# Optimization experiments

Hardware: AMD Instinct MI355X
Metric: run time of the kernel (lower is better)

Reference implementation:

```python
import jax, jax.numpy as jnp
import numpy as np

H, DK = 8, 64  # n_head, d_k (= d_v)
LN_EPS = 1e-6


def _layer_norm(x, g, b):
    mu = jnp.mean(x, axis=-1, keepdims=True)
    var = jnp.var(x, axis=-1, keepdims=True)
    return (x - mu) * jax.lax.rsqrt(var + LN_EPS) * g + b


def setup_inputs() -> dict:
    key = jax.random.key(0)
    ks = jax.random.split(key, 8)
    B, S, D, DF = 8, 1024, 512, 2048
    s = 0.02
    return {
        "enc_input": jax.random.normal(ks[0], (B, S, D), jnp.float32),
        "cost_mat": jax.random.normal(ks[1], (B, S, S), jnp.float32),
        "wq": jax.random.normal(ks[2], (D, D), jnp.float32) * s,
        "wk": jax.random.normal(ks[3], (D, D), jnp.float32) * s,
        "wv": jax.random.normal(ks[4], (D, D), jnp.float32) * s,
        "fc_w": jax.random.normal(ks[5], (D, D), jnp.float32) * s,
        "ln1_g": jnp.ones((D,), jnp.float32),
        "ln1_b": jnp.zeros((D,), jnp.float32),
        "w1": jax.random.normal(ks[6], (DF, D), jnp.float32) * s,
        "b1": jnp.zeros((DF,), jnp.float32),
        "w2": jax.random.normal(ks[7], (D, DF), jnp.float32) * s,
        "b2": jnp.zeros((D,), jnp.float32),
        "ln2_g": jnp.ones((D,), jnp.float32),
        "ln2_b": jnp.zeros((D,), jnp.float32),
    }


def reference(enc_input, cost_mat, wq, wk, wv, fc_w, ln1_g, ln1_b,
              w1, b1, w2, b2, ln2_g, ln2_b):
    B, S, D = enc_input.shape
    # Q/K/V projections -> [B, H, S, dk]
    q = (enc_input @ wq.T).reshape(B, S, H, DK).transpose(0, 2, 1, 3)
    k = (enc_input @ wk.T).reshape(B, S, H, DK).transpose(0, 2, 1, 3)
    v = (enc_input @ wv.T).reshape(B, S, H, DK).transpose(0, 2, 1, 3)
    # mixed score: scaled QK^T plus cost matrix broadcast over heads
    scores = jnp.einsum("bhqd,bhkd->bhqk", q, k) / np.sqrt(DK).astype(np.float32)
    scores = scores + cost_mat[:, None, :, :]
    attn = jax.nn.softmax(scores, axis=-1)
    ctx = jnp.einsum("bhqk,bhkd->bhqd", attn, v)  # [B,H,S,dk]
    ctx = ctx.transpose(0, 2, 1, 3).reshape(B, S, D)
    attn_out = _layer_norm(ctx @ fc_w.T + enc_input, ln1_g, ln1_b)
    # position-wise FFN with residual + layernorm
    h = jax.nn.relu(attn_out @ w1.T + b1)
    ffn = h @ w2.T + b2
    return _layer_norm(ffn + attn_out, ln2_g, ln2_b)
```

## Files before the change

kernel.cpp:

```cpp
#include <hip/hip_runtime.h>
#include <stdint.h>

typedef __attribute__((ext_vector_type(8))) short bf16x8;
typedef __attribute__((ext_vector_type(4))) float f32x4;

__device__ __forceinline__ unsigned short f2bf(float f) {
  unsigned int u = __builtin_bit_cast(unsigned int, f);
  u += 0x7fffu + ((u >> 16) & 1u);
  return (unsigned short)(u >> 16);
}

__device__ __forceinline__ float bf2f(unsigned short u) {
  unsigned int x = ((unsigned int)u) << 16;
  return __builtin_bit_cast(float, x);
}

__device__ __forceinline__ void gload16(const void* g, void* l) {
  __builtin_amdgcn_global_load_lds(
      (const __attribute__((address_space(1))) void*)g,
      (__attribute__((address_space(3))) void*)l, 16, 0, 0);
}

__device__ __forceinline__ int xcd_remap(int i, int nwg) {
  return (i & 7) * (nwg >> 3) + (i >> 3);
}

__global__ void cvt_all(const float* __restrict__ enc,
                        const float* __restrict__ cost,
                        const float* __restrict__ wq,
                        const float* __restrict__ wk,
                        const float* __restrict__ wv,
                        const float* __restrict__ fcw,
                        const float* __restrict__ w1,
                        const float* __restrict__ w2,
                        unsigned short* __restrict__ enc_bf,
                        unsigned short* __restrict__ cost_bf,
                        unsigned short* __restrict__ wqkv_bf,
                        unsigned short* __restrict__ fcw_bf,
                        unsigned short* __restrict__ w1_bf,
                        unsigned short* __restrict__ w2_bf) {
  const int i = blockIdx.x * 256 + threadIdx.x;
  constexpr int E0 = 1048576;
  constexpr int E1 = E0 + 2097152;
  constexpr int E2 = E1 + 65536;
  constexpr int E3 = E2 + 65536;
  constexpr int E4 = E3 + 65536;
  constexpr int E5 = E4 + 65536;
  constexpr int E6 = E5 + 262144;
  constexpr int E7 = E6 + 262144;
  const float* in;
  unsigned short* out;
  int base;
  float scale = 1.0f;
  if (i < E0)      { in = enc;  out = enc_bf;            base = 0;  }
  else if (i < E1) { in = cost; out = cost_bf;           base = E0; scale = 1.44269504f; }
  else if (i < E2) { in = wq;   out = wqkv_bf;           base = E1; }
  else if (i < E3) { in = wk;   out = wqkv_bf + 262144;  base = E2; }
  else if (i < E4) { in = wv;   out = wqkv_bf + 524288;  base = E3; }
  else if (i < E5) { in = fcw;  out = fcw_bf;            base = E4; }
  else if (i < E6) { in = w1;   out = w1_bf;             base = E5; }
  else if (i < E7) { in = w2;   out = w2_bf;             base = E6; }
  else return;
  const int k = i - base;
  float4 v = ((const float4*)in)[k];
  ushort4 o;
  o.x = f2bf(v.x * scale);
  o.y = f2bf(v.y * scale);
  o.z = f2bf(v.z * scale);
  o.w = f2bf(v.w * scale);
  ((ushort4*)out)[k] = o;
}

template <int EPI>
__global__ __launch_bounds__(256, 2) void gemm_bt(
    const unsigned short* __restrict__ A, const unsigned short* __restrict__ B,
    void* __restrict__ C, const float* __restrict__ bias, int M, int N, int K) {
  __shared__ unsigned short Al[2][128 * 32];
  __shared__ unsigned short Bl[2][128 * 32];
  const int tid = threadIdx.x;
  const int lane = tid & 63;
  const int wid = tid >> 6;
  const int wr = wid >> 1;
  const int wc = wid & 1;
  const int nwg = gridDim.x * gridDim.y;
  const int j_ = xcd_remap(blockIdx.y * gridDim.x + blockIdx.x, nwg);
  const int m0 = (j_ / gridDim.x) * 128;
  const int n0 = (j_ % gridDim.x) * 128;

  f32x4 acc[4][4];
#pragma unroll
  for (int i = 0; i < 4; ++i)
#pragma unroll
    for (int j = 0; j < 4; ++j) acc[i][j] = f32x4{0.f, 0.f, 0.f, 0.f};

  const int srow = wid * 32 + (lane >> 2);
  const int scol = (lane & 3) * 8;
  const unsigned short* Ag = A + (size_t)(m0 + srow) * K + scol;
  const unsigned short* Bg = B + (size_t)(n0 + srow) * K + scol;
  const size_t K16 = (size_t)16 * K;

  auto stage = [&](int buf, int kt) {
    unsigned short* Ald = &Al[buf][wid * 1024];
    unsigned short* Bld = &Bl[buf][wid * 1024];
    gload16(Ag + kt, Ald);
    gload16(Ag + K16 + kt, Ald + 512);
    gload16(Bg + kt, Bld);
    gload16(Bg + K16 + kt, Bld + 512);
  };

  const int ko = (lane >> 4) * 8;
  const int arow = wr * 64 + (lane & 15);
  const int brow = wc * 64 + (lane & 15);

  stage(0, 0);
  __syncthreads();
  for (int kt = 0, it = 0; kt < K; kt += 32, ++it) {
    const int cur = it & 1;
    if (kt + 32 < K) stage(cur ^ 1, kt + 32);
    bf16x8 af[4], bf[4];
#pragma unroll
    for (int mi = 0; mi < 4; ++mi)
      af[mi] = *(const bf16x8*)&Al[cur][(arow + mi * 16) * 32 + ko];
#pragma unroll
    for (int ni = 0; ni < 4; ++ni)
      bf[ni] = *(const bf16x8*)&Bl[cur][(brow + ni * 16) * 32 + ko];
#pragma unroll
    for (int mi = 0; mi < 4; ++mi)
#pragma unroll
      for (int ni = 0; ni < 4; ++ni)
        acc[mi][ni] = __builtin_amdgcn_mfma_f32_16x16x32_bf16(
            af[mi], bf[ni], acc[mi][ni], 0, 0, 0);
    __syncthreads();
  }

  const int rl = (lane >> 4) * 4;
  const int cl = lane & 15;
#pragma unroll
  for (int mi = 0; mi < 4; ++mi) {
#pragma unroll
    for (int ni = 0; ni < 4; ++ni) {
      const int r0 = m0 + wr * 64 + mi * 16 + rl;
      const int c = n0 + wc * 64 + ni * 16 + cl;
      if (EPI == 5 && c >= 1024) {
        unsigned short* Vt = (unsigned short*)C + (size_t)2 * 8192 * 512;
        const int cc = c - 1024;
        ushort4 pk;
        pk.x = f2bf(acc[mi][ni][0]);
        pk.y = f2bf(acc[mi][ni][1]);
        pk.z = f2bf(acc[mi][ni][2]);
        pk.w = f2bf(acc[mi][ni][3]);
        const int b_ = r0 >> 10, s_ = r0 & 1023, h_ = cc >> 6, dd = cc & 63;
        *(ushort4*)(Vt + ((size_t)((b_ * 8 + h_) * 64 + dd) * 1024 + s_)) = pk;
      } else if (EPI == 5) {
        unsigned short* dst =
            (c < 512) ? (unsigned short*)C + (size_t)r0 * 512 + c
                      : (unsigned short*)C + (size_t)8192 * 512 +
                            (size_t)r0 * 512 + (c - 512);
#pragma unroll
        for (int j = 0; j < 4; ++j) dst[(size_t)j * 512] = f2bf(acc[mi][ni][j]);
      } else {
#pragma unroll
        for (int j = 0; j < 4; ++j) {
          float v = acc[mi][ni][j];
          if (EPI == 2) v = fmaxf(v + bias[c], 0.f);
          ((unsigned short*)C)[(size_t)(r0 + j) * N + c] = f2bf(v);
        }
      }
    }
  }
}

template <int EPI>
__global__ __launch_bounds__(256, 2) void gemm_bt64(
    const unsigned short* __restrict__ A, const unsigned short* __restrict__ B,
    void* __restrict__ C, const float* __restrict__ bias, int M, int N, int K) {
  __shared__ unsigned short Al[2][64 * 64];
  __shared__ unsigned short Bl[2][128 * 64];
  const int tid = threadIdx.x;
  const int lane = tid & 63;
  const int wid = tid >> 6;
  const int nwg = gridDim.x * gridDim.y;
  const int j_ = xcd_remap(blockIdx.y * gridDim.x + blockIdx.x, nwg);
  const int m0 = (j_ / gridDim.x) * 64;
  const int n0 = (j_ % gridDim.x) * 128;

  f32x4 acc[4][2];
#pragma unroll
  for (int i = 0; i < 4; ++i)
#pragma unroll
    for (int j = 0; j < 2; ++j) acc[i][j] = f32x4{0.f, 0.f, 0.f, 0.f};

  const int srow = tid >> 3;
  const int scol = ((tid & 7) * 8) ^ ((srow & 7) * 8);
  const unsigned short* Ag = A + (size_t)(m0 + srow) * K + scol;
  const unsigned short* Bg = B + (size_t)(n0 + srow) * K + scol;

  auto stage = [&](int buf, int kt) {
#pragma unroll
    for (int i = 0; i < 2; ++i)
      gload16(Ag + (size_t)(32 * i) * K + kt, &Al[buf][wid * 512 + i * 2048]);
#pragma unroll
    for (int i = 0; i < 4; ++i)
      gload16(Bg + (size_t)(32 * i) * K + kt, &Bl[buf][wid * 512 + i * 2048]);
  };

  const int ko = (lane >> 4) * 8;
  const int cl16 = lane & 15;
  const int fswz = (cl16 & 7) * 8;

  stage(0, 0);
  __syncthreads();
  for (int kt = 0, it = 0; kt < K; kt += 64, ++it) {
    const int cur = it & 1;
    if (kt + 64 < K) stage(cur ^ 1, kt + 64);
#pragma unroll
    for (int kh = 0; kh < 2; ++kh) {
      bf16x8 af[4], bf[2];
#pragma unroll
      for (int mi = 0; mi < 4; ++mi)
        af[mi] = *(const bf16x8*)&Al[cur][(mi * 16 + cl16) * 64 +
                                          ((kh * 32 + ko) ^ fswz)];
#pragma unroll
      for (int ni = 0; ni < 2; ++ni)
        bf[ni] = *(const bf16x8*)&Bl[cur][(wid * 32 + ni * 16 + cl16) * 64 +
                                          ((kh * 32 + ko) ^ fswz)];
#pragma unroll
      for (int mi = 0; mi < 4; ++mi)
#pragma unroll
        for (int ni = 0; ni < 2; ++ni)
          acc[mi][ni] = __builtin_amdgcn_mfma_f32_16x16x32_bf16(
              af[mi], bf[ni], acc[mi][ni], 0, 0, 0);
    }
    __syncthreads();
  }

  const int rl = (lane >> 4) * 4;
#pragma unroll
  for (int mi = 0; mi < 4; ++mi) {
#pragma unroll
    for (int ni = 0; ni < 2; ++ni) {
      const int r0 = m0 + mi * 16 + rl;
      const int c = n0 + wid * 32 + ni * 16 + cl16;
#pragma unroll
      for (int j = 0; j < 4; ++j) {
        float v = acc[mi][ni][j];
        if (EPI == 6) v += bias[c];
        ((unsigned short*)C)[(size_t)(r0 + j) * N + c] = f2bf(v);
      }
    }
  }
}

__global__ __launch_bounds__(512, 4) void attn_kernel(
    const unsigned short* __restrict__ Q, const unsigned short* __restrict__ K,
    const unsigned short* __restrict__ V,
    const unsigned short* __restrict__ Cb,
    unsigned short* __restrict__ ctx) {
  __shared__ unsigned short Kl[2][4096];
  __shared__ unsigned short Vl[2][4096];
  __shared__ unsigned short Cl[2][8192];
  __shared__ unsigned short P[8][1024];
  const int tid = threadIdx.x, lane = tid & 63, wid = tid >> 6;
  const int j_ = xcd_remap(blockIdx.y * 8 + blockIdx.x, 512);
  const int bh = j_ >> 3, b = bh >> 3, h = bh & 7;
  const int q0 = (j_ & 7) * 128;
  const int qw = q0 + wid * 16;
  const int cl = lane & 15, gl = lane >> 4;

  const unsigned short* qp =
      Q + (size_t)(b * 1024 + qw + cl) * 512 + h * 64 + gl * 8;
  const bf16x8 qf0 = *(const bf16x8*)qp;
  const bf16x8 qf1 = *(const bf16x8*)(qp + 32);

  f32x4 acc[4];
  float lsum = 0.f;
#pragma unroll
  for (int i = 0; i < 4; ++i) acc[i] = f32x4{0.f, 0.f, 0.f, 0.f};

  const int srow = tid >> 3;
  const int swzc = ((tid & 7) * 8) ^ ((srow & 7) << 3);
  const unsigned short* Ksrc =
      K + (size_t)(b * 1024 + srow) * 512 + h * 64 + swzc;
  const unsigned short* Vsrc = V + (size_t)(bh * 64 + srow) * 1024 + swzc;
  const unsigned short* Csrc =
      Cb + (size_t)(b * 1024 + q0 + srow) * 1024 + swzc;

  auto stage_all = [&](int buf, int k0) {
    gload16(Ksrc + (size_t)k0 * 512, &Kl[buf][wid * 512]);
    gload16(Vsrc + k0, &Vl[buf][wid * 512]);
    gload16(Csrc + k0, &Cl[buf][wid * 512]);
    gload16(Csrc + (size_t)64 * 1024 + k0, &Cl[buf][4096 + wid * 512]);
  };

  const int ks = (cl & 7) << 3;
  const int pswz = (cl & 7) << 3;
  const int crow = wid * 16 + cl;

  stage_all(0, 0);
  __syncthreads();

  for (int t = 0; t < 16; ++t) {
    const int cur = t & 1;
    if (t < 15) stage_all(cur ^ 1, (t + 1) * 64);

#pragma unroll
    for (int ni = 0; ni < 4; ++ni) {
      const int krow = ni * 16 + cl;
      bf16x8 k0f = *(const bf16x8*)&Kl[cur][krow * 64 + ((gl * 8) ^ ks)];
      bf16x8 k1f = *(const bf16x8*)&Kl[cur][krow * 64 + ((32 + gl * 8) ^ ks)];
      f32x4 t2 = f32x4{0.f, 0.f, 0.f, 0.f};
      t2 = __builtin_amdgcn_mfma_f32_16x16x32_bf16(k0f, qf0, t2, 0, 0, 0);
      t2 = __builtin_amdgcn_mfma_f32_16x16x32_bf16(k1f, qf1, t2, 0, 0, 0);
      const uint2 cpk =
          *(const uint2*)&Cl[cur][crow * 64 + ((ni * 16 + gl * 4) ^ pswz)];
      float p0, p1, p2, p3;
      {
        float e0 = __builtin_fmaf(t2[0], 0.18033688f, bf2f((unsigned short)(cpk.x & 0xffff)));
        float e1 = __builtin_fmaf(t2[1], 0.18033688f, bf2f((unsigned short)(cpk.x >> 16)));
        float e2 = __builtin_fmaf(t2[2], 0.18033688f, bf2f((unsigned short)(cpk.y & 0xffff)));
        float e3 = __builtin_fmaf(t2[3], 0.18033688f, bf2f((unsigned short)(cpk.y >> 16)));
        asm("v_exp_f32 %0, %1" : "=v"(p0) : "v"(e0));
        asm("v_exp_f32 %0, %1" : "=v"(p1) : "v"(e1));
        asm("v_exp_f32 %0, %1" : "=v"(p2) : "v"(e2));
        asm("v_exp_f32 %0, %1" : "=v"(p3) : "v"(e3));
      }
      lsum += (p0 + p1) + (p2 + p3);
      uint32_t lo, hi;
      asm("v_cvt_pk_bf16_f32 %0, %1, %2" : "=v"(lo) : "v"(p0), "v"(p1));
      asm("v_cvt_pk_bf16_f32 %0, %1, %2" : "=v"(hi) : "v"(p2), "v"(p3));
      *(uint2*)&P[wid][cl * 64 + ((ni * 16 + gl * 4) ^ pswz)] = uint2{lo, hi};
    }

    bf16x8 pf0 = *(const bf16x8*)&P[wid][cl * 64 + ((gl * 8) ^ pswz)];
    bf16x8 pf1 = *(const bf16x8*)&P[wid][cl * 64 + ((32 + gl * 8) ^ pswz)];
#pragma unroll
    for (int nv = 0; nv < 4; ++nv) {
      const int vrow = nv * 16 + cl;
      bf16x8 v0f = *(const bf16x8*)&Vl[cur][vrow * 64 + ((gl * 8) ^ ks)];
      bf16x8 v1f = *(const bf16x8*)&Vl[cur][vrow * 64 + ((32 + gl * 8) ^ ks)];
      acc[nv] =
          __builtin_amdgcn_mfma_f32_16x16x32_bf16(pf0, v0f, acc[nv], 0, 0, 0);
      acc[nv] =
          __builtin_amdgcn_mfma_f32_16x16x32_bf16(pf1, v1f, acc[nv], 0, 0, 0);
    }
    __syncthreads();
  }

  lsum += __shfl_xor(lsum, 16);
  lsum += __shfl_xor(lsum, 32);
  const float linv = 1.0f / lsum;
  float linvw[4];
#pragma unroll
  for (int j = 0; j < 4; ++j) linvw[j] = __shfl(linv, gl * 4 + j);
#pragma unroll
  for (int nv = 0; nv < 4; ++nv)
#pragma unroll
    for (int j = 0; j < 4; ++j) {
      float v = acc[nv][j] * linvw[j];
      ctx[(size_t)(b * 1024 + qw + gl * 4 + j) * 512 + h * 64 + nv * 16 + cl] =
          f2bf(v);
    }
}

template <int OUT_F32>
__global__ __launch_bounds__(256) void ln_kernel(
    const unsigned short* __restrict__ x1, const unsigned short* __restrict__ x2,
    const float* __restrict__ g, const float* __restrict__ bt,
    void* __restrict__ out) {
  const int lane = threadIdx.x & 63, wid = threadIdx.x >> 6;
  const int row = blockIdx.x * 4 + wid;
  const bf16x8 a = *(const bf16x8*)(x1 + (size_t)row * 512 + lane * 8);
  const bf16x8 bb = *(const bf16x8*)(x2 + (size_t)row * 512 + lane * 8);
  float x[8];
#pragma unroll
  for (int i = 0; i < 8; ++i)
    x[i] = bf2f((unsigned short)a[i]) + bf2f((unsigned short)bb[i]);
  float sum = 0.f, sq = 0.f;
#pragma unroll
  for (int i = 0; i < 8; ++i) {
    sum += x[i];
    sq += x[i] * x[i];
  }
#pragma unroll
  for (int m = 1; m <= 32; m <<= 1) {
    sum += __shfl_xor(sum, m);
    sq += __shfl_xor(sq, m);
  }
  const float mean = sum * (1.f / 512.f);
  const float var = sq * (1.f / 512.f) - mean * mean;
  const float rstd = rsqrtf(var + 1e-6f);
  float y[8];
#pragma unroll
  for (int i = 0; i < 8; ++i) {
    const int c = lane * 8 + i;
    y[i] = (x[i] - mean) * rstd * g[c] + bt[c];
  }
  if (OUT_F32) {
    float4* op = (float4*)((float*)out + (size_t)row * 512);
    op[lane * 2] = make_float4(y[0], y[1], y[2], y[3]);
    op[lane * 2 + 1] = make_float4(y[4], y[5], y[6], y[7]);
  } else {
    bf16x8 o;
#pragma unroll
    for (int i = 0; i < 8; ++i) o[i] = (short)f2bf(y[i]);
    *(bf16x8*)((unsigned short*)out + (size_t)row * 512 + lane * 8) = o;
  }
}

extern "C" void kernel_launch(void* const* d_in, const int* in_sizes, int n_in,
                              void* d_out, int out_size, void* d_ws,
                              size_t ws_size, hipStream_t stream) {
  const float* enc = (const float*)d_in[0];
  const float* cost = (const float*)d_in[1];
  const float* wq = (const float*)d_in[2];
  const float* wk = (const float*)d_in[3];
  const float* wv = (const float*)d_in[4];
  const float* fcw = (const float*)d_in[5];
  const float* ln1g = (const float*)d_in[6];
  const float* ln1b = (const float*)d_in[7];
  const float* w1 = (const float*)d_in[8];
  const float* b1 = (const float*)d_in[9];
  const float* w2 = (const float*)d_in[10];
  const float* b2 = (const float*)d_in[11];
  const float* ln2g = (const float*)d_in[12];
  const float* ln2b = (const float*)d_in[13];

  char* ws = (char*)d_ws;
  size_t off = 0;
  auto alloc = [&](size_t n) {
    void* p = ws + off;
    off += (n + 255) & ~(size_t)255;
    return p;
  };
  const size_t MD = 8192ull * 512;
  const size_t MF = 8192ull * 2048;
  unsigned short* enc_bf = (unsigned short*)alloc(MD * 2);
  unsigned short* wqkv_bf = (unsigned short*)alloc(3 * 512 * 512 * 2);
  unsigned short* fcw_bf = (unsigned short*)alloc(512 * 512 * 2);
  unsigned short* w1_bf = (unsigned short*)alloc(2048 * 512 * 2);
  unsigned short* w2_bf = (unsigned short*)alloc(512 * 2048 * 2);
  unsigned short* Qb = (unsigned short*)alloc(MD * 2 * 3);
  unsigned short* Kb = Qb + MD;
  unsigned short* Vt = Kb + MD;
  unsigned short* ctx_bf = (unsigned short*)alloc(MD * 2);
  unsigned short* fc_bf = (unsigned short*)alloc(MD * 2);
  unsigned short* attn_bf = (unsigned short*)alloc(MD * 2);
  unsigned short* ffn_bf = (unsigned short*)alloc(MD * 2);
  unsigned short* h_bf = (unsigned short*)alloc(MF * 2);
  unsigned short* cost_bf = h_bf;

  cvt_all<<<15360, 256, 0, stream>>>(enc, cost, wq, wk, wv, fcw, w1, w2,
                                     enc_bf, cost_bf, wqkv_bf, fcw_bf, w1_bf,
                                     w2_bf);

  gemm_bt<5><<<dim3(12, 64), 256, 0, stream>>>(enc_bf, wqkv_bf, Qb, nullptr,
                                               8192, 1536, 512);
  attn_kernel<<<dim3(8, 64), 512, 0, stream>>>(Qb, Kb, Vt, cost_bf, ctx_bf);
  gemm_bt64<0><<<dim3(4, 128), 256, 0, stream>>>(ctx_bf, fcw_bf, fc_bf,
                                                 nullptr, 8192, 512, 512);
  ln_kernel<0><<<2048, 256, 0, stream>>>(fc_bf, enc_bf, ln1g, ln1b, attn_bf);
  gemm_bt<2><<<dim3(16, 64), 256, 0, stream>>>(attn_bf, w1_bf, h_bf, b1, 8192,
                                               2048, 512);
  gemm_bt64<6><<<dim3(4, 128), 256, 0, stream>>>(h_bf, w2_bf, ffn_bf, b2, 8192,
                                                 512, 2048);
  ln_kernel<1><<<2048, 256, 0, stream>>>(ffn_bf, attn_bf, ln2g, ln2b, d_out);
}
```

Baseline: 143.5 us.

## Double GEMM K-tile to 64 with XOR-swizzled LDS layout

Raises the GEMM K-tile per stage from 32 to 64, so there are half as many main-loop iterations and __syncthreads barriers per output tile. The LDS tile is also restaged with an XOR swizzle on the column offset, applied on both the global-to-LDS load and the fragment reads, to avoid bank conflicts on the wider 64-element rows. LDS use doubles to 64 KB per block, which may limit occupancy below the launch bound of two blocks per CU.

```diff
diff --git a/kernel.cpp b/kernel.cpp
--- a/kernel.cpp
+++ b/kernel.cpp
@@ -75,8 +75,8 @@
 __global__ __launch_bounds__(256, 2) void gemm_bt(
     const unsigned short* __restrict__ A, const unsigned short* __restrict__ B,
     void* __restrict__ C, const float* __restrict__ bias, int M, int N, int K) {
-  __shared__ unsigned short Al[2][128 * 32];
-  __shared__ unsigned short Bl[2][128 * 32];
+  __shared__ unsigned short Al[2][128 * 64];
+  __shared__ unsigned short Bl[2][128 * 64];
   const int tid = threadIdx.x;
   const int lane = tid & 63;
   const int wid = tid >> 6;
@@ -93,48 +93,53 @@
 #pragma unroll
     for (int j = 0; j < 4; ++j) acc[i][j] = f32x4{0.f, 0.f, 0.f, 0.f};
 
-  const int srow = wid * 32 + (lane >> 2);
-  const int scol = (lane & 3) * 8;
+  const int srow = tid >> 3;
+  const int scol = ((tid & 7) * 8) ^ ((srow & 7) * 8);
   const unsigned short* Ag = A + (size_t)(m0 + srow) * K + scol;
   const unsigned short* Bg = B + (size_t)(n0 + srow) * K + scol;
-  const size_t K16 = (size_t)16 * K;
 
   auto stage = [&](int buf, int kt) {
-    unsigned short* Ald = &Al[buf][wid * 1024];
-    unsigned short* Bld = &Bl[buf][wid * 1024];
-    gload16(Ag + kt, Ald);
-    gload16(Ag + K16 + kt, Ald + 512);
-    gload16(Bg + kt, Bld);
-    gload16(Bg + K16 + kt, Bld + 512);
+#pragma unroll
+    for (int i = 0; i < 4; ++i)
+      gload16(Ag + (size_t)(32 * i) * K + kt, &Al[buf][wid * 512 + i * 2048]);
+#pragma unroll
+    for (int i = 0; i < 4; ++i)
+      gload16(Bg + (size_t)(32 * i) * K + kt, &Bl[buf][wid * 512 + i * 2048]);
   };
 
   const int ko = (lane >> 4) * 8;
-  const int arow = wr * 64 + (lane & 15);
-  const int brow = wc * 64 + (lane & 15);
+  const int cl = lane & 15;
+  const int arow = wr * 64 + cl;
+  const int brow = wc * 64 + cl;
+  const int fswz = (cl & 7) * 8;
 
   stage(0, 0);
   __syncthreads();
-  for (int kt = 0, it = 0; kt < K; kt += 32, ++it) {
+  for (int kt = 0, it = 0; kt < K; kt += 64, ++it) {
     const int cur = it & 1;
-    if (kt + 32 < K) stage(cur ^ 1, kt + 32);
-    bf16x8 af[4], bf[4];
-#pragma unroll
-    for (int mi = 0; mi < 4; ++mi)
-      af[mi] = *(const bf16x8*)&Al[cur][(arow + mi * 16) * 32 + ko];
-#pragma unroll
-    for (int ni = 0; ni < 4; ++ni)
-      bf[ni] = *(const bf16x8*)&Bl[cur][(brow + ni * 16) * 32 + ko];
-#pragma unroll
-    for (int mi = 0; mi < 4; ++mi)
+    if (kt + 64 < K) stage(cur ^ 1, kt + 64);
+#pragma unroll
+    for (int kh = 0; kh < 2; ++kh) {
+      bf16x8 af[4], bf[4];
+#pragma unroll
+      for (int mi = 0; mi < 4; ++mi)
+        af[mi] = *(const bf16x8*)&Al[cur][(arow + mi * 16) * 64 +
+                                          ((kh * 32 + ko) ^ fswz)];
 #pragma unroll
       for (int ni = 0; ni < 4; ++ni)
-        acc[mi][ni] = __builtin_amdgcn_mfma_f32_16x16x32_bf16(
-            af[mi], bf[ni], acc[mi][ni], 0, 0, 0);
+        bf[ni] = *(const bf16x8*)&Bl[cur][(brow + ni * 16) * 64 +
+                                          ((kh * 32 + ko) ^ fswz)];
+#pragma unroll
+      for (int mi = 0; mi < 4; ++mi)
+#pragma unroll
+        for (int ni = 0; ni < 4; ++ni)
+          acc[mi][ni] = __builtin_amdgcn_mfma_f32_16x16x32_bf16(
+              af[mi], bf[ni], acc[mi][ni], 0, 0, 0);
+    }
     __syncthreads();
   }
 
   const int rl = (lane >> 4) * 4;
-  const int cl = lane & 15;
 #pragma unroll
   for (int mi = 0; mi < 4; ++mi) {
 #pragma unroll
```

New measurement: 150.5 us. +4.9%, slower.
